# Performance work log

Measured on AMD Instinct MI355X. Metric: run time of the kernel, lower is better.

## Reference

```python
import jax, jax.numpy as jnp
import numpy as np


def setup_inputs() -> dict:
    key = jax.random.key(0)
    k1, k2 = jax.random.split(key)
    group, bs, channels = 16, 16384, 128
    x = jax.random.normal(k1, (group, bs, channels), dtype=jnp.float32)
    weight = jax.random.normal(k2, (group, channels, channels), dtype=jnp.float32)
    return {"x": x, "weight": weight}


def reference(x, weight):
    """Sequential Householder reflection composition.

    x:      (group, m, n)
    weight: (group, n, channels) with channels == n; column i is the i-th reflector.
    Each step: x <- x - 2/(w^T w) * (x w) w^T  with w = weight[:, :, i].
    """
    # (channels, group, n): reflector for each scan step
    ws = jnp.moveaxis(weight, -1, 0)

    def step(xc, w):
        # w: (group, n)
        denom = jnp.sum(w * w, axis=-1)[:, None]            # (group, 1)
        xw = jnp.einsum('gmn,gn->gm', xc, w)                # (group, m)
        coef = (2.0 * xw) / denom                           # (group, m)
        xc = xc - coef[:, :, None] * w[:, None, :]          # (group, m, n)
        return xc, None

    out, _ = jax.lax.scan(step, x, ws)
    return out
```

## Files before the change

### kernel.cpp

```cpp
#include <hip/hip_runtime.h>
#include <stdint.h>

typedef __attribute__((ext_vector_type(8))) short short8;
typedef __attribute__((ext_vector_type(4))) float f32x4;
typedef unsigned short u16;

#define GROUPS 16
#define MROWS  16384
#define NCH    128

__device__ __forceinline__ u16 f2bf(float f) {
    uint32_t u = __float_as_uint(f);
    u += 0x7FFFu + ((u >> 16) & 1u);
    return (u16)(u >> 16);
}

__global__ __launch_bounds__(256) void build_q(const float* __restrict__ w,
                                               u16* __restrict__ qt) {
    __shared__ float wt[128 * 128];
    const int g   = blockIdx.y;
    const int rb  = blockIdx.x;
    const int tid = threadIdx.x;
    const float* wg = w + (size_t)g * NCH * NCH;

    const int ci = tid & 127;
    float den = 0.f;
    for (int r = 0; r < 128; r += 4) {
        float a0 = wg[(r + 0) * 128 + ci];
        float a1 = wg[(r + 1) * 128 + ci];
        float a2 = wg[(r + 2) * 128 + ci];
        float a3 = wg[(r + 3) * 128 + ci];
        den += a0 * a0 + a1 * a1 + a2 * a2 + a3 * a3;
    }
    if (tid < 128) wt[tid] = sqrtf(2.0f / den);
    __syncthreads();
    const float scl = wt[ci];
    __syncthreads();

    {
        const int h = tid >> 7;
        for (int p = 0; p < 64; ++p) {
            int r = 2 * p + h;
            wt[ci * 128 + ((r + 4 * ci) & 127)] = wg[r * 128 + ci] * scl;
        }
    }
    __syncthreads();

    const int t = rb * 16 + (tid >> 4);
    const int s = tid & 15;
    float q[8];
#pragma unroll
    for (int u = 0; u < 2; ++u)
#pragma unroll
        for (int e = 0; e < 4; ++e)
            q[u * 4 + e] = (4 * s + 64 * u + e == t) ? 1.0f : 0.0f;

    const f32x4* wt4 = (const f32x4*)wt;
    for (int i = 0; i < 128; ++i) {
        f32x4 v0 = wt4[i * 32 + ((s + 0  + i) & 31)];
        f32x4 v1 = wt4[i * 32 + ((s + 16 + i) & 31)];
        float pa = q[0] * v0.x + q[1] * v0.y + q[2] * v0.z + q[3] * v0.w;
        float pb = q[4] * v1.x + q[5] * v1.y + q[6] * v1.z + q[7] * v1.w;
        pa += pb;
        pa += __shfl_xor(pa, 1);
        pa += __shfl_xor(pa, 2);
        pa += __shfl_xor(pa, 4);
        pa += __shfl_xor(pa, 8);
        q[0] -= pa * v0.x; q[1] -= pa * v0.y; q[2] -= pa * v0.z; q[3] -= pa * v0.w;
        q[4] -= pa * v1.x; q[5] -= pa * v1.y; q[6] -= pa * v1.z; q[7] -= pa * v1.w;
    }

    u16* qg = qt + (size_t)g * NCH * NCH;
#pragma unroll
    for (int u = 0; u < 2; ++u)
#pragma unroll
        for (int e = 0; e < 4; ++e)
            qg[(4 * s + 64 * u + e) * 128 + t] = f2bf(q[u * 4 + e]);
}

__global__ __launch_bounds__(256) void apply_q(const float* __restrict__ x,
                                               const u16* __restrict__ qt,
                                               float* __restrict__ out) {
    __shared__ __align__(16) u16 qs[16][128][8];
    const int g   = blockIdx.y;
    const int bx  = blockIdx.x;
    const int tid = threadIdx.x;
    const int wv  = tid >> 6;
    const int l   = tid & 63;
    const int lr  = l & 15;
    const int lb  = l >> 4;

    const size_t rowidx = (size_t)g * MROWS + (size_t)bx * 64 + wv * 16 + lr;
    const float* xlane = x   + rowidx * NCH;
    float*       olane = out + rowidx * NCH;

    f32x4 xa[8];
#pragma unroll
    for (int kb = 0; kb < 4; ++kb) {
        xa[kb * 2 + 0] = *(const f32x4*)(xlane + kb * 32 + lb * 8);
        xa[kb * 2 + 1] = *(const f32x4*)(xlane + kb * 32 + lb * 8 + 4);
    }

    const u16* qg = qt + (size_t)g * NCH * NCH;
#pragma unroll
    for (int p = 0; p < 8; ++p) {
        int f = tid + 256 * p;
        int c = f & 127;
        int s = f >> 7;
        *(uint4*)(&qs[s][c][0]) = *(const uint4*)(qg + c * 128 + s * 8);
    }
    __syncthreads();

    short8 afr[4];
#pragma unroll
    for (int kb = 0; kb < 4; ++kb) {
        f32x4 v0 = xa[kb * 2], v1 = xa[kb * 2 + 1];
        short8 a;
        a[0] = (short)f2bf(v0.x); a[1] = (short)f2bf(v0.y);
        a[2] = (short)f2bf(v0.z); a[3] = (short)f2bf(v0.w);
        a[4] = (short)f2bf(v1.x); a[5] = (short)f2bf(v1.y);
        a[6] = (short)f2bf(v1.z); a[7] = (short)f2bf(v1.w);
        afr[kb] = a;
    }

    f32x4 acc[8];
#pragma unroll
    for (int nt = 0; nt < 8; ++nt) { f32x4 z = {0.f, 0.f, 0.f, 0.f}; acc[nt] = z; }

#pragma unroll
    for (int kb = 0; kb < 4; ++kb) {
        const int s = kb * 4 + lb;
#pragma unroll
        for (int nt = 0; nt < 8; ++nt) {
            short8 qf = *(const short8*)(&qs[s][nt * 16 + lr][0]);
            acc[nt] = __builtin_amdgcn_mfma_f32_16x16x32_bf16(qf, afr[kb], acc[nt], 0, 0, 0);
        }
    }

#pragma unroll
    for (int nt = 0; nt < 8; ++nt)
        *(f32x4*)(olane + nt * 16 + lb * 4) = acc[nt];
}

extern "C" void kernel_launch(void* const* d_in, const int* in_sizes, int n_in,
                              void* d_out, int out_size, void* d_ws, size_t ws_size,
                              hipStream_t stream) {
    const float* x = (const float*)d_in[0];
    const float* w = (const float*)d_in[1];
    float* out = (float*)d_out;
    u16* qtw = (u16*)d_ws;

    build_q<<<dim3(8, GROUPS), 256, 0, stream>>>(w, qtw);
    apply_q<<<dim3(MROWS / 64, GROUPS), 256, 0, stream>>>(x, qtw, out);
}
```

Baseline: 89.09 us.

## Process two row tiles per block and load Q directly into LDS

Each apply_q block now handles 128 rows instead of 64. Both row tiles' x loads are issued up front, and the staged bf16 Q matrix in LDS is reused across two MFMA passes. Q staging uses global_load_lds to copy straight into shared memory without going through registers, and launch bounds request 4 blocks per CU. This halves the number of blocks and the per-block Q staging, but it doubles the x register footprint, which may reduce occupancy or cause spills.

```diff
diff --git a/kernel.cpp b/kernel.cpp
--- a/kernel.cpp
+++ b/kernel.cpp
@@ -78,9 +78,9 @@
             qg[(4 * s + 64 * u + e) * 128 + t] = f2bf(q[u * 4 + e]);
 }
 
-__global__ __launch_bounds__(256) void apply_q(const float* __restrict__ x,
-                                               const u16* __restrict__ qt,
-                                               float* __restrict__ out) {
+__global__ __launch_bounds__(256, 4) void apply_q(const float* __restrict__ x,
+                                                  const u16* __restrict__ qt,
+                                                  float* __restrict__ out) {
     __shared__ __align__(16) u16 qs[16][128][8];
     const int g   = blockIdx.y;
     const int bx  = blockIdx.x;
@@ -90,56 +90,94 @@
     const int lr  = l & 15;
     const int lb  = l >> 4;
 
-    const size_t rowidx = (size_t)g * MROWS + (size_t)bx * 64 + wv * 16 + lr;
-    const float* xlane = x   + rowidx * NCH;
-    float*       olane = out + rowidx * NCH;
+    const size_t row0 = (size_t)g * MROWS + (size_t)bx * 128 + wv * 16 + lr;
+    const float* xlane = x   + row0 * NCH;
+    float*       olane = out + row0 * NCH;
 
-    f32x4 xa[8];
+    f32x4 x0[8], x1[8];
 #pragma unroll
     for (int kb = 0; kb < 4; ++kb) {
-        xa[kb * 2 + 0] = *(const f32x4*)(xlane + kb * 32 + lb * 8);
-        xa[kb * 2 + 1] = *(const f32x4*)(xlane + kb * 32 + lb * 8 + 4);
+        x0[2 * kb + 0] = *(const f32x4*)(xlane + kb * 32 + lb * 8);
+        x0[2 * kb + 1] = *(const f32x4*)(xlane + kb * 32 + lb * 8 + 4);
+    }
+#pragma unroll
+    for (int kb = 0; kb < 4; ++kb) {
+        x1[2 * kb + 0] = *(const f32x4*)(xlane + 64 * NCH + kb * 32 + lb * 8);
+        x1[2 * kb + 1] = *(const f32x4*)(xlane + 64 * NCH + kb * 32 + lb * 8 + 4);
     }
 
     const u16* qg = qt + (size_t)g * NCH * NCH;
+    {
+        char* lbase = (char*)&qs[0][0][0];
 #pragma unroll
-    for (int p = 0; p < 8; ++p) {
-        int f = tid + 256 * p;
-        int c = f & 127;
-        int s = f >> 7;
-        *(uint4*)(&qs[s][c][0]) = *(const uint4*)(qg + c * 128 + s * 8);
+        for (int p = 0; p < 8; ++p) {
+            int f = tid + 256 * p;
+            const char* src = (const char*)qg + (f & 127) * 256 + (f >> 7) * 16;
+            __builtin_amdgcn_global_load_lds(
+                (const __attribute__((address_space(1))) void*)src,
+                (__attribute__((address_space(3))) void*)(lbase + f * 16),
+                16, 0, 0);
+        }
     }
     __syncthreads();
 
-    short8 afr[4];
+    {
+        short8 afr[4];
 #pragma unroll
-    for (int kb = 0; kb < 4; ++kb) {
-        f32x4 v0 = xa[kb * 2], v1 = xa[kb * 2 + 1];
-        short8 a;
-        a[0] = (short)f2bf(v0.x); a[1] = (short)f2bf(v0.y);
-        a[2] = (short)f2bf(v0.z); a[3] = (short)f2bf(v0.w);
-        a[4] = (short)f2bf(v1.x); a[5] = (short)f2bf(v1.y);
-        a[6] = (short)f2bf(v1.z); a[7] = (short)f2bf(v1.w);
-        afr[kb] = a;
+        for (int kb = 0; kb < 4; ++kb) {
+            f32x4 v0 = x0[2 * kb], v1 = x0[2 * kb + 1];
+            short8 a;
+            a[0] = (short)f2bf(v0.x); a[1] = (short)f2bf(v0.y);
+            a[2] = (short)f2bf(v0.z); a[3] = (short)f2bf(v0.w);
+            a[4] = (short)f2bf(v1.x); a[5] = (short)f2bf(v1.y);
+            a[6] = (short)f2bf(v1.z); a[7] = (short)f2bf(v1.w);
+            afr[kb] = a;
+        }
+        f32x4 acc[8];
+#pragma unroll
+        for (int nt = 0; nt < 8; ++nt) { f32x4 z = {0.f, 0.f, 0.f, 0.f}; acc[nt] = z; }
+#pragma unroll
+        for (int kb = 0; kb < 4; ++kb) {
+            const int s = kb * 4 + lb;
+#pragma unroll
+            for (int nt = 0; nt < 8; ++nt) {
+                short8 qf = *(const short8*)(&qs[s][nt * 16 + lr][0]);
+                acc[nt] = __builtin_amdgcn_mfma_f32_16x16x32_bf16(qf, afr[kb], acc[nt], 0, 0, 0);
+            }
+        }
+#pragma unroll
+        for (int nt = 0; nt < 8; ++nt)
+            *(f32x4*)(olane + nt * 16 + lb * 4) = acc[nt];
     }
 
-    f32x4 acc[8];
+    {
+        short8 afr[4];
 #pragma unroll
-    for (int nt = 0; nt < 8; ++nt) { f32x4 z = {0.f, 0.f, 0.f, 0.f}; acc[nt] = z; }
-
+        for (int kb = 0; kb < 4; ++kb) {
+            f32x4 v0 = x1[2 * kb], v1 = x1[2 * kb + 1];
+            short8 a;
+            a[0] = (short)f2bf(v0.x); a[1] = (short)f2bf(v0.y);
+            a[2] = (short)f2bf(v0.z); a[3] = (short)f2bf(v0.w);
+            a[4] = (short)f2bf(v1.x); a[5] = (short)f2bf(v1.y);
+            a[6] = (short)f2bf(v1.z); a[7] = (short)f2bf(v1.w);
+            afr[kb] = a;
+        }
+        f32x4 acc[8];
 #pragma unroll
-    for (int kb = 0; kb < 4; ++kb) {
-        const int s = kb * 4 + lb;
+        for (int nt = 0; nt < 8; ++nt) { f32x4 z = {0.f, 0.f, 0.f, 0.f}; acc[nt] = z; }
 #pragma unroll
-        for (int nt = 0; nt < 8; ++nt) {
-            short8 qf = *(const short8*)(&qs[s][nt * 16 + lr][0]);
-            acc[nt] = __builtin_amdgcn_mfma_f32_16x16x32_bf16(qf, afr[kb], acc[nt], 0, 0, 0);
+        for (int kb = 0; kb < 4; ++kb) {
+            const int s = kb * 4 + lb;
+#pragma unroll
+            for (int nt = 0; nt < 8; ++nt) {
+                short8 qf = *(const short8*)(&qs[s][nt * 16 + lr][0]);
+                acc[nt] = __builtin_amdgcn_mfma_f32_16x16x32_bf16(qf, afr[kb], acc[nt], 0, 0, 0);
+            }
         }
+#pragma unroll
+        for (int nt = 0; nt < 8; ++nt)
+            *(f32x4*)(olane + 64 * NCH + nt * 16 + lb * 4) = acc[nt];
     }
-
-#pragma unroll
-    for (int nt = 0; nt < 8; ++nt)
-        *(f32x4*)(olane + nt * 16 + lb * 4) = acc[nt];
 }
 
 extern "C" void kernel_launch(void* const* d_in, const int* in_sizes, int n_in,
@@ -151,5 +189,5 @@
     u16* qtw = (u16*)d_ws;
 
     build_q<<<dim3(8, GROUPS), 256, 0, stream>>>(w, qtw);
-    apply_q<<<dim3(MROWS / 64, GROUPS), 256, 0, stream>>>(x, qtw, out);
+    apply_q<<<dim3(MROWS / 128, GROUPS), 256, 0, stream>>>(x, qtw, out);
 }
```

After: 90.55 us. No clear change (+1.6%).
